# Kernel tuning notes

Hardware: AMD Instinct MI355X
Metric: run time of the kernel (lower is better)

## Reference

```python
import jax, jax.numpy as jnp
import numpy as np

N_QUBITS = 4
INV_SQRT2 = np.float32(1.0 / np.sqrt(2.0))
CNOT_PAIRS = [(0, 1), (1, 2), (2, 3), (3, 0), (0, 2), (1, 3), (2, 0), (3, 1)]


def _apply_1q(state, U, w):
    # state: (B,2,2,2,2); U: (B,2,2) batched or (2,2) shared
    state = jnp.moveaxis(state, w + 1, 1)
    if U.ndim == 3:
        state = jnp.einsum('bij,bj...->bi...', U, state)
    else:
        state = jnp.einsum('ij,bj...->bi...', U, state)
    return jnp.moveaxis(state, 1, w + 1)


def _apply_cnot(state, c, t):
    st = jnp.moveaxis(state, (c + 1, t + 1), (1, 2))
    st = jnp.stack([st[:, 0], st[:, 1, ::-1]], axis=1)  # flip target where ctrl=1
    return jnp.moveaxis(st, (1, 2), (c + 1, t + 1))


def _ry_batched(theta):  # theta: (B,) -> (B,2,2) complex
    c, s = jnp.cos(theta * 0.5), jnp.sin(theta * 0.5)
    return jnp.stack([jnp.stack([c, -s], -1), jnp.stack([s, c], -1)], -2).astype(jnp.complex64)


def _rz_batched(theta):  # theta: (B,) -> (B,2,2) complex (diag(e^{-i t/2}, e^{i t/2}))
    e = jnp.exp(-0.5j * theta.astype(jnp.complex64))
    z = jnp.zeros_like(e)
    return jnp.stack([jnp.stack([e, z], -1), jnp.stack([z, jnp.conj(e)], -1)], -2)


def _ry1(t):  # scalar -> (2,2)
    c, s = jnp.cos(t * 0.5), jnp.sin(t * 0.5)
    return jnp.stack([jnp.stack([c, -s]), jnp.stack([s, c])]).astype(jnp.complex64)


def _rz1(t):  # scalar -> (2,2)
    e = jnp.exp(-0.5j * t.astype(jnp.complex64))
    z = jnp.zeros_like(e)
    return jnp.stack([jnp.stack([e, z]), jnp.stack([z, jnp.conj(e)])])


def _circuit(f, weights):
    # f: (B, 4) angle features; weights: (L, 4, 3). Returns <Z_i> per wire: (B, 4).
    B = f.shape[0]
    state = jnp.zeros((B, 2, 2, 2, 2), jnp.complex64).at[:, 0, 0, 0, 0].set(1.0)
    H = jnp.array([[1.0, 1.0], [1.0, -1.0]], jnp.complex64) * INV_SQRT2
    for i in range(N_QUBITS):
        state = _apply_1q(state, H, i)
        state = _apply_1q(state, _ry_batched(jnp.arctan(f[:, i])), i)
        state = _apply_1q(state, _rz_batched(jnp.arctan(f[:, i] ** 2)), i)
    n_layers = weights.shape[0]
    for l in range(n_layers):
        for c, t in CNOT_PAIRS:
            state = _apply_cnot(state, c, t)
        for i in range(N_QUBITS):
            phi, theta, omega = weights[l, i, 0], weights[l, i, 1], weights[l, i, 2]
            # PennyLane Rot(phi, theta, omega) = RZ(omega) @ RY(theta) @ RZ(phi)
            U = _rz1(omega) @ _ry1(theta) @ _rz1(phi)
            state = _apply_1q(state, U, i)
    probs = jnp.abs(state) ** 2  # (B,2,2,2,2)
    z = []
    for i in range(N_QUBITS):
        axes = tuple(a for a in range(1, N_QUBITS + 1) if a != i + 1)
        m = probs.sum(axes)  # (B,2)
        z.append(m[:, 0] - m[:, 1])
    return jnp.stack(z, -1)


def setup_inputs() -> dict:
    key = jax.random.key(0)
    ks = jax.random.split(key, 6)
    B, D_IN, D_OUT, L = 131072, 256, 64, 2
    x = jax.random.normal(ks[0], (B, D_IN), jnp.float32)
    W1 = jax.random.normal(ks[1], (N_QUBITS, D_IN), jnp.float32) * (1.0 / np.sqrt(D_IN))
    b1 = jax.random.normal(ks[2], (N_QUBITS,), jnp.float32) * 0.1
    weights = jax.random.normal(ks[3], (L, N_QUBITS, 3), jnp.float32)
    W2 = jax.random.normal(ks[4], (D_OUT, N_QUBITS), jnp.float32) * 0.5
    b2 = jax.random.normal(ks[5], (D_OUT,), jnp.float32) * 0.1
    return {"x": x, "W1": W1, "b1": b1, "weights": weights, "W2": W2, "b2": b2}


def reference(x, W1, b1, weights, W2, b2):
    f = jnp.tanh(x @ W1.T + b1) * jnp.pi  # (B,4)
    q = _circuit(f, weights)              # (B,4) expval(PauliZ)
    return q @ W2.T + b2                  # (B, D_OUT)
```

## Files before the change

### kernel.cpp

```cpp
#include <hip/hip_runtime.h>
#include <math.h>

#define NQ 4
#define DIN 256
#define DOUT 64
#define NLAYER 2
#define TPB 256
#define WROWS 64
#define NIT (WROWS/2)
#define PF 3

typedef float nt4 __attribute__((ext_vector_type(4)));

__device__ __forceinline__ float tanh_fast(float y) {
    float e = __expf(2.0f * y);
    return 1.0f - 2.0f / (e + 1.0f);
}

__global__ __launch_bounds__(TPB, 2) void qp_fused(
    const float* __restrict__ x,  const float* __restrict__ W1,
    const float* __restrict__ b1, const float* __restrict__ wts,
    const float* __restrict__ W2, const float* __restrict__ b2,
    float* __restrict__ out)
{
    __shared__ __align__(16) float fs[4][WROWS][NQ];
    __shared__ __align__(16) float qs[4][WROWS][NQ];
    __shared__ __align__(16) float w2s[DOUT][NQ];
    __shared__ __align__(16) float us[8][8];
    __shared__ float b2s[DOUT];

    const int t = threadIdx.x;
    const int wave = t >> 6, lane = t & 63;
    const int half = lane >> 5;
    const int cl   = lane & 31;
    const int qsel = lane & 3;

    if (t < 64) {
        ((float4*)&w2s[0][0])[t] = ((const float4*)W2)[t];
        b2s[t] = b2[t];
    }
    if (t < 8) {
        const float phi = wts[t*3 + 0], th = wts[t*3 + 1], om = wts[t*3 + 2];
        float sth, cth; sincosf(0.5f*th, &sth, &cth);
        float sp, cp;   sincosf(0.5f*(phi+om), &sp, &cp);
        float sm, cm;   sincosf(0.5f*(phi-om), &sm, &cm);
        us[t][0] =  cth*cp; us[t][1] = -cth*sp;
        us[t][2] = -sth*cm; us[t][3] = -sth*sm;
        us[t][4] =  sth*cm; us[t][5] = -sth*sm;
        us[t][6] =  cth*cp; us[t][7] =  cth*sp;
    }
    __syncthreads();

    const int wrow = (blockIdx.x * 4 + wave) * WROWS;
    float (* __restrict__ fsw)[NQ] = fs[wave];
    float (* __restrict__ qsw)[NQ] = qs[wave];

    {
        float4 w[4][2];
        #pragma unroll
        for (int q = 0; q < 4; ++q) {
            w[q][0] = ((const float4*)W1)[q*64 + cl];
            w[q][1] = ((const float4*)W1)[q*64 + 32 + cl];
        }
        const float4 bv = *(const float4*)b1;
        const float bsel = (qsel==0)?bv.x:(qsel==1)?bv.y:(qsel==2)?bv.z:bv.w;

        const int row0 = wrow + half;

        nt4 buf[PF+1][2];
        #pragma unroll
        for (int k = 0; k < PF; ++k) {
            const nt4* xn = (const nt4*)(x + (size_t)(row0 + k*2) * DIN);
            buf[k][0] = __builtin_nontemporal_load(xn + cl);
            buf[k][1] = __builtin_nontemporal_load(xn + 32 + cl);
        }

        #pragma unroll
        for (int it = 0; it < NIT; ++it) {
            if (it + PF < NIT) {
                const nt4* xn = (const nt4*)(x + (size_t)(row0 + (it+PF)*2) * DIN);
                buf[(it+PF)&PF][0] = __builtin_nontemporal_load(xn + cl);
                buf[(it+PF)&PF][1] = __builtin_nontemporal_load(xn + 32 + cl);
            }
            const nt4 xv0 = buf[it&PF][0];
            const nt4 xv1 = buf[it&PF][1];

            float a0, a1, a2, a3;
            a0 = fmaf(xv0.x,w[0][0].x, fmaf(xv0.y,w[0][0].y, fmaf(xv0.z,w[0][0].z, xv0.w*w[0][0].w)));
            a1 = fmaf(xv0.x,w[1][0].x, fmaf(xv0.y,w[1][0].y, fmaf(xv0.z,w[1][0].z, xv0.w*w[1][0].w)));
            a2 = fmaf(xv0.x,w[2][0].x, fmaf(xv0.y,w[2][0].y, fmaf(xv0.z,w[2][0].z, xv0.w*w[2][0].w)));
            a3 = fmaf(xv0.x,w[3][0].x, fmaf(xv0.y,w[3][0].y, fmaf(xv0.z,w[3][0].z, xv0.w*w[3][0].w)));
            a0 = fmaf(xv1.x,w[0][1].x, fmaf(xv1.y,w[0][1].y, fmaf(xv1.z,w[0][1].z, fmaf(xv1.w,w[0][1].w, a0))));
            a1 = fmaf(xv1.x,w[1][1].x, fmaf(xv1.y,w[1][1].y, fmaf(xv1.z,w[1][1].z, fmaf(xv1.w,w[1][1].w, a1))));
            a2 = fmaf(xv1.x,w[2][1].x, fmaf(xv1.y,w[2][1].y, fmaf(xv1.z,w[2][1].z, fmaf(xv1.w,w[2][1].w, a2))));
            a3 = fmaf(xv1.x,w[3][1].x, fmaf(xv1.y,w[3][1].y, fmaf(xv1.z,w[3][1].z, fmaf(xv1.w,w[3][1].w, a3))));

            a0 += __shfl_xor(a0, 1, 64);  a1 += __shfl_xor(a1, 1, 64);
            a2 += __shfl_xor(a2, 1, 64);  a3 += __shfl_xor(a3, 1, 64);
            a0 += __shfl_xor(a0, 2, 64);  a1 += __shfl_xor(a1, 2, 64);
            a2 += __shfl_xor(a2, 2, 64);  a3 += __shfl_xor(a3, 2, 64);
            float v = (qsel==0)?a0:(qsel==1)?a1:(qsel==2)?a2:a3;
            v += __shfl_xor(v, 4, 64);
            v += __shfl_xor(v, 8, 64);
            v += __shfl_xor(v, 16, 64);

            if (cl < 4) {
                const float PI = 3.14159265358979f;
                fsw[it*2 + half][qsel] = PI * tanh_fast(v + bsel);
            }
        }
    }

    {
        const float4 fv = *(const float4*)fsw[lane];
        const float fq[4] = {fv.x, fv.y, fv.z, fv.w};
        const float IS2 = 0.70710678118654752f;
        float vr[4][2], vi[4][2];
        #pragma unroll
        for (int i = 0; i < 4; ++i) {
            const float fi = fq[i];
            const float f2 = fi*fi;
            const float ca = rsqrtf(1.0f + f2);
            const float ch = sqrtf(0.5f*(1.0f + ca));
            const float sh = copysignf(sqrtf(fmaxf(0.5f*(1.0f - ca), 0.0f)), fi);
            const float cb = rsqrtf(1.0f + f2*f2);
            const float cbh = sqrtf(0.5f*(1.0f + cb));
            const float sbh = sqrtf(fmaxf(0.5f*(1.0f - cb), 0.0f));
            const float u0 = (ch - sh) * IS2;
            const float u1 = (ch + sh) * IS2;
            vr[i][0] = u0 * cbh;  vi[i][0] = -u0 * sbh;
            vr[i][1] = u1 * cbh;  vi[i][1] =  u1 * sbh;
        }
        float ar[16], ai[16];
        #pragma unroll
        for (int i0 = 0; i0 < 2; ++i0)
        #pragma unroll
        for (int i1 = 0; i1 < 2; ++i1) {
            const float pr  = vr[0][i0]*vr[1][i1] - vi[0][i0]*vi[1][i1];
            const float pim = vr[0][i0]*vi[1][i1] + vi[0][i0]*vr[1][i1];
            #pragma unroll
            for (int i2 = 0; i2 < 2; ++i2)
            #pragma unroll
            for (int i3 = 0; i3 < 2; ++i3) {
                const float qr  = vr[2][i2]*vr[3][i3] - vi[2][i2]*vi[3][i3];
                const float qim = vr[2][i2]*vi[3][i3] + vi[2][i2]*vr[3][i3];
                const int idx = i0*8 + i1*4 + i2*2 + i3;
                ar[idx] = pr*qr - pim*qim;
                ai[idx] = pr*qim + pim*qr;
            }
        }
        #pragma unroll
        for (int l = 0; l < NLAYER; ++l) {
            constexpr int cpairs[8][2] = {{0,1},{1,2},{2,3},{3,0},{0,2},{1,3},{2,0},{3,1}};
            #pragma unroll
            for (int g = 0; g < 8; ++g) {
                const int bc = 8 >> cpairs[g][0];
                const int bt = 8 >> cpairs[g][1];
                #pragma unroll
                for (int m = 0; m < 16; ++m) {
                    if ((m & bc) && !(m & bt)) {
                        const int m2 = m | bt;
                        float tr = ar[m]; ar[m] = ar[m2]; ar[m2] = tr;
                        float ti = ai[m]; ai[m] = ai[m2]; ai[m2] = ti;
                    }
                }
            }
            #pragma unroll
            for (int i = 0; i < 4; ++i) {
                const float* u = &us[l*4 + i][0];
                const float u00r=u[0], u00i=u[1], u01r=u[2], u01i=u[3];
                const float u10r=u[4], u10i=u[5], u11r=u[6], u11i=u[7];
                const int bq = 8 >> i;
                #pragma unroll
                for (int m = 0; m < 16; ++m) {
                    if (!(m & bq)) {
                        const int m2 = m | bq;
                        const float a0r=ar[m], a0i=ai[m], a1r=ar[m2], a1i=ai[m2];
                        ar[m]  = u00r*a0r - u00i*a0i + u01r*a1r - u01i*a1i;
                        ai[m]  = u00r*a0i + u00i*a0r + u01r*a1i + u01i*a1r;
                        ar[m2] = u10r*a0r - u10i*a0i + u11r*a1r - u11i*a1i;
                        ai[m2] = u10r*a0i + u10i*a0r + u11r*a1i + u11i*a1r;
                    }
                }
            }
        }
        float z0=0.f, z1=0.f, z2=0.f, z3=0.f;
        #pragma unroll
        for (int m = 0; m < 16; ++m) {
            const float p = ar[m]*ar[m] + ai[m]*ai[m];
            z0 += (m & 8) ? -p : p;
            z1 += (m & 4) ? -p : p;
            z2 += (m & 2) ? -p : p;
            z3 += (m & 1) ? -p : p;
        }
        float4 qv; qv.x=z0; qv.y=z1; qv.z=z2; qv.w=z3;
        *(float4*)qsw[lane] = qv;
    }

    {
        const int j4 = lane & 15;
        const int rb = lane >> 4;
        float w2r[4][4], b2r[4];
        #pragma unroll
        for (int jj = 0; jj < 4; ++jj) {
            const int j = j4*4 + jj;
            #pragma unroll
            for (int i = 0; i < 4; ++i) w2r[jj][i] = w2s[j][i];
            b2r[jj] = b2s[j];
        }
        #pragma unroll
        for (int e = 0; e < WROWS/4; ++e) {
            const int r = e*4 + rb;
            const float4 q = *(const float4*)qsw[r];
            nt4 o;
            o.x = fmaf(q.x,w2r[0][0], fmaf(q.y,w2r[0][1], fmaf(q.z,w2r[0][2], fmaf(q.w,w2r[0][3], b2r[0]))));
            o.y = fmaf(q.x,w2r[1][0], fmaf(q.y,w2r[1][1], fmaf(q.z,w2r[1][2], fmaf(q.w,w2r[1][3], b2r[1]))));
            o.z = fmaf(q.x,w2r[2][0], fmaf(q.y,w2r[2][1], fmaf(q.z,w2r[2][2], fmaf(q.w,w2r[2][3], b2r[2]))));
            o.w = fmaf(q.x,w2r[3][0], fmaf(q.y,w2r[3][1], fmaf(q.z,w2r[3][2], fmaf(q.w,w2r[3][3], b2r[3]))));
            __builtin_nontemporal_store(o, (nt4*)(out + (size_t)(wrow + r) * DOUT) + j4);
        }
    }
}

extern "C" void kernel_launch(void* const* d_in, const int* in_sizes, int n_in,
                              void* d_out, int out_size, void* d_ws, size_t ws_size,
                              hipStream_t stream) {
    const float* x  = (const float*)d_in[0];
    const float* W1 = (const float*)d_in[1];
    const float* b1 = (const float*)d_in[2];
    const float* wt = (const float*)d_in[3];
    const float* W2 = (const float*)d_in[4];
    const float* b2 = (const float*)d_in[5];
    float* out = (float*)d_out;
    const int B = in_sizes[0] / DIN;
    qp_fused<<<B / (WROWS * 4), TPB, 0, stream>>>(x, W1, b1, wt, W2, b2, out);
}
```

Before: 35.67 us.

## Split fused kernel into separate projection and circuit/output kernels

Splits the single fused kernel into two launches. The first streams x and computes the tanh projection into a workspace buffer (or into the output buffer as scratch), using many more, smaller blocks. The second does the circuit simulation with one row per thread and the output projection. This raises parallelism and occupancy for the memory-bound read of x and for the compute phase, at the cost of a second launch and an extra global round trip for the features.

```diff
diff --git a/kernel.cpp b/kernel.cpp
--- a/kernel.cpp
+++ b/kernel.cpp
@@ -6,9 +6,8 @@
 #define DOUT 64
 #define NLAYER 2
 #define TPB 256
-#define WROWS 64
-#define NIT (WROWS/2)
 #define PF 3
+#define K1_NIT 8
 
 typedef float nt4 __attribute__((ext_vector_type(4)));
 
@@ -17,28 +16,83 @@
     return 1.0f - 2.0f / (e + 1.0f);
 }
 
-__global__ __launch_bounds__(TPB, 2) void qp_fused(
-    const float* __restrict__ x,  const float* __restrict__ W1,
-    const float* __restrict__ b1, const float* __restrict__ wts,
-    const float* __restrict__ W2, const float* __restrict__ b2,
-    float* __restrict__ out)
+__global__ __launch_bounds__(TPB, 4) void qp_k1(
+    const float* __restrict__ x, const float* __restrict__ W1,
+    const float* __restrict__ b1, float* __restrict__ fbuf, int fstride)
 {
-    __shared__ __align__(16) float fs[4][WROWS][NQ];
-    __shared__ __align__(16) float qs[4][WROWS][NQ];
-    __shared__ __align__(16) float w2s[DOUT][NQ];
-    __shared__ __align__(16) float us[8][8];
-    __shared__ float b2s[DOUT];
-
     const int t = threadIdx.x;
     const int wave = t >> 6, lane = t & 63;
     const int half = lane >> 5;
     const int cl   = lane & 31;
     const int qsel = lane & 3;
 
-    if (t < 64) {
-        ((float4*)&w2s[0][0])[t] = ((const float4*)W2)[t];
-        b2s[t] = b2[t];
-    }
+    float4 w[4][2];
+    #pragma unroll
+    for (int q = 0; q < 4; ++q) {
+        w[q][0] = ((const float4*)W1)[q*64 + cl];
+        w[q][1] = ((const float4*)W1)[q*64 + 32 + cl];
+    }
+    const float4 bv = *(const float4*)b1;
+    const float bsel = (qsel==0)?bv.x:(qsel==1)?bv.y:(qsel==2)?bv.z:bv.w;
+
+    const int wrow = blockIdx.x * 64 + wave * 16;
+    const int row0 = wrow + half;
+
+    nt4 buf[PF+1][2];
+    #pragma unroll
+    for (int k = 0; k < PF; ++k) {
+        const nt4* xn = (const nt4*)(x + (size_t)(row0 + k*2) * DIN);
+        buf[k][0] = __builtin_nontemporal_load(xn + cl);
+        buf[k][1] = __builtin_nontemporal_load(xn + 32 + cl);
+    }
+
+    #pragma unroll
+    for (int it = 0; it < K1_NIT; ++it) {
+        if (it + PF < K1_NIT) {
+            const nt4* xn = (const nt4*)(x + (size_t)(row0 + (it+PF)*2) * DIN);
+            buf[(it+PF)&PF][0] = __builtin_nontemporal_load(xn + cl);
+            buf[(it+PF)&PF][1] = __builtin_nontemporal_load(xn + 32 + cl);
+        }
+        const nt4 xv0 = buf[it&PF][0];
+        const nt4 xv1 = buf[it&PF][1];
+
+        float a0, a1, a2, a3;
+        a0 = fmaf(xv0.x,w[0][0].x, fmaf(xv0.y,w[0][0].y, fmaf(xv0.z,w[0][0].z, xv0.w*w[0][0].w)));
+        a1 = fmaf(xv0.x,w[1][0].x, fmaf(xv0.y,w[1][0].y, fmaf(xv0.z,w[1][0].z, xv0.w*w[1][0].w)));
+        a2 = fmaf(xv0.x,w[2][0].x, fmaf(xv0.y,w[2][0].y, fmaf(xv0.z,w[2][0].z, xv0.w*w[2][0].w)));
+        a3 = fmaf(xv0.x,w[3][0].x, fmaf(xv0.y,w[3][0].y, fmaf(xv0.z,w[3][0].z, xv0.w*w[3][0].w)));
+        a0 = fmaf(xv1.x,w[0][1].x, fmaf(xv1.y,w[0][1].y, fmaf(xv1.z,w[0][1].z, fmaf(xv1.w,w[0][1].w, a0))));
+        a1 = fmaf(xv1.x,w[1][1].x, fmaf(xv1.y,w[1][1].y, fmaf(xv1.z,w[1][1].z, fmaf(xv1.w,w[1][1].w, a1))));
+        a2 = fmaf(xv1.x,w[2][1].x, fmaf(xv1.y,w[2][1].y, fmaf(xv1.z,w[2][1].z, fmaf(xv1.w,w[2][1].w, a2))));
+        a3 = fmaf(xv1.x,w[3][1].x, fmaf(xv1.y,w[3][1].y, fmaf(xv1.z,w[3][1].z, fmaf(xv1.w,w[3][1].w, a3))));
+
+        a0 += __shfl_xor(a0, 1, 64);  a1 += __shfl_xor(a1, 1, 64);
+        a2 += __shfl_xor(a2, 1, 64);  a3 += __shfl_xor(a3, 1, 64);
+        a0 += __shfl_xor(a0, 2, 64);  a1 += __shfl_xor(a1, 2, 64);
+        a2 += __shfl_xor(a2, 2, 64);  a3 += __shfl_xor(a3, 2, 64);
+        float v = (qsel==0)?a0:(qsel==1)?a1:(qsel==2)?a2:a3;
+        v += __shfl_xor(v, 4, 64);
+        v += __shfl_xor(v, 8, 64);
+        v += __shfl_xor(v, 16, 64);
+
+        if (cl < 4) {
+            const float PI = 3.14159265358979f;
+            fbuf[(size_t)(row0 + it*2) * fstride + qsel] = PI * tanh_fast(v + bsel);
+        }
+    }
+}
+
+__global__ __launch_bounds__(TPB, 4) void qp_k2(
+    const float* __restrict__ fbuf, int fstride,
+    const float* __restrict__ wts, const float* __restrict__ W2,
+    const float* __restrict__ b2, float* __restrict__ out)
+{
+    __shared__ __align__(16) float qs[TPB][NQ];
+    __shared__ __align__(16) float us[8][8];
+
+    const int t = threadIdx.x;
+    const int brow = blockIdx.x * TPB;
+
     if (t < 8) {
         const float phi = wts[t*3 + 0], th = wts[t*3 + 1], om = wts[t*3 + 2];
         float sth, cth; sincosf(0.5f*th, &sth, &cth);
@@ -51,68 +105,8 @@
     }
     __syncthreads();
 
-    const int wrow = (blockIdx.x * 4 + wave) * WROWS;
-    float (* __restrict__ fsw)[NQ] = fs[wave];
-    float (* __restrict__ qsw)[NQ] = qs[wave];
-
     {
-        float4 w[4][2];
-        #pragma unroll
-        for (int q = 0; q < 4; ++q) {
-            w[q][0] = ((const float4*)W1)[q*64 + cl];
-            w[q][1] = ((const float4*)W1)[q*64 + 32 + cl];
-        }
-        const float4 bv = *(const float4*)b1;
-        const float bsel = (qsel==0)?bv.x:(qsel==1)?bv.y:(qsel==2)?bv.z:bv.w;
-
-        const int row0 = wrow + half;
-
-        nt4 buf[PF+1][2];
-        #pragma unroll
-        for (int k = 0; k < PF; ++k) {
-            const nt4* xn = (const nt4*)(x + (size_t)(row0 + k*2) * DIN);
-            buf[k][0] = __builtin_nontemporal_load(xn + cl);
-            buf[k][1] = __builtin_nontemporal_load(xn + 32 + cl);
-        }
-
-        #pragma unroll
-        for (int it = 0; it < NIT; ++it) {
-            if (it + PF < NIT) {
-                const nt4* xn = (const nt4*)(x + (size_t)(row0 + (it+PF)*2) * DIN);
-                buf[(it+PF)&PF][0] = __builtin_nontemporal_load(xn + cl);
-                buf[(it+PF)&PF][1] = __builtin_nontemporal_load(xn + 32 + cl);
-            }
-            const nt4 xv0 = buf[it&PF][0];
-            const nt4 xv1 = buf[it&PF][1];
-
-            float a0, a1, a2, a3;
-            a0 = fmaf(xv0.x,w[0][0].x, fmaf(xv0.y,w[0][0].y, fmaf(xv0.z,w[0][0].z, xv0.w*w[0][0].w)));
-            a1 = fmaf(xv0.x,w[1][0].x, fmaf(xv0.y,w[1][0].y, fmaf(xv0.z,w[1][0].z, xv0.w*w[1][0].w)));
-            a2 = fmaf(xv0.x,w[2][0].x, fmaf(xv0.y,w[2][0].y, fmaf(xv0.z,w[2][0].z, xv0.w*w[2][0].w)));
-            a3 = fmaf(xv0.x,w[3][0].x, fmaf(xv0.y,w[3][0].y, fmaf(xv0.z,w[3][0].z, xv0.w*w[3][0].w)));
-            a0 = fmaf(xv1.x,w[0][1].x, fmaf(xv1.y,w[0][1].y, fmaf(xv1.z,w[0][1].z, fmaf(xv1.w,w[0][1].w, a0))));
-            a1 = fmaf(xv1.x,w[1][1].x, fmaf(xv1.y,w[1][1].y, fmaf(xv1.z,w[1][1].z, fmaf(xv1.w,w[1][1].w, a1))));
-            a2 = fmaf(xv1.x,w[2][1].x, fmaf(xv1.y,w[2][1].y, fmaf(xv1.z,w[2][1].z, fmaf(xv1.w,w[2][1].w, a2))));
-            a3 = fmaf(xv1.x,w[3][1].x, fmaf(xv1.y,w[3][1].y, fmaf(xv1.z,w[3][1].z, fmaf(xv1.w,w[3][1].w, a3))));
-
-            a0 += __shfl_xor(a0, 1, 64);  a1 += __shfl_xor(a1, 1, 64);
-            a2 += __shfl_xor(a2, 1, 64);  a3 += __shfl_xor(a3, 1, 64);
-            a0 += __shfl_xor(a0, 2, 64);  a1 += __shfl_xor(a1, 2, 64);
-            a2 += __shfl_xor(a2, 2, 64);  a3 += __shfl_xor(a3, 2, 64);
-            float v = (qsel==0)?a0:(qsel==1)?a1:(qsel==2)?a2:a3;
-            v += __shfl_xor(v, 4, 64);
-            v += __shfl_xor(v, 8, 64);
-            v += __shfl_xor(v, 16, 64);
-
-            if (cl < 4) {
-                const float PI = 3.14159265358979f;
-                fsw[it*2 + half][qsel] = PI * tanh_fast(v + bsel);
-            }
-        }
-    }
-
-    {
-        const float4 fv = *(const float4*)fsw[lane];
+        const float4 fv = *(const float4*)(fbuf + (size_t)(brow + t) * fstride);
         const float fq[4] = {fv.x, fv.y, fv.z, fv.w};
         const float IS2 = 0.70710678118654752f;
         float vr[4][2], vi[4][2];
@@ -194,30 +188,28 @@
             z3 += (m & 1) ? -p : p;
         }
         float4 qv; qv.x=z0; qv.y=z1; qv.z=z2; qv.w=z3;
-        *(float4*)qsw[lane] = qv;
-    }
+        ((float4*)qs)[t] = qv;
+    }
+    __syncthreads();
 
     {
-        const int j4 = lane & 15;
-        const int rb = lane >> 4;
-        float w2r[4][4], b2r[4];
-        #pragma unroll
-        for (int jj = 0; jj < 4; ++jj) {
-            const int j = j4*4 + jj;
-            #pragma unroll
-            for (int i = 0; i < 4; ++i) w2r[jj][i] = w2s[j][i];
-            b2r[jj] = b2s[j];
-        }
-        #pragma unroll
-        for (int e = 0; e < WROWS/4; ++e) {
-            const int r = e*4 + rb;
-            const float4 q = *(const float4*)qsw[r];
+        const int j4 = t & 15;
+        const int rb = t >> 4;
+        float4 w2r[4];
+        #pragma unroll
+        for (int jj = 0; jj < 4; ++jj) w2r[jj] = ((const float4*)W2)[j4*4 + jj];
+        const float4 b2v = ((const float4*)b2)[j4];
+
+        #pragma unroll
+        for (int e = 0; e < TPB/16; ++e) {
+            const int r = e*16 + rb;
+            const float4 q = ((const float4*)qs)[r];
             nt4 o;
-            o.x = fmaf(q.x,w2r[0][0], fmaf(q.y,w2r[0][1], fmaf(q.z,w2r[0][2], fmaf(q.w,w2r[0][3], b2r[0]))));
-            o.y = fmaf(q.x,w2r[1][0], fmaf(q.y,w2r[1][1], fmaf(q.z,w2r[1][2], fmaf(q.w,w2r[1][3], b2r[1]))));
-            o.z = fmaf(q.x,w2r[2][0], fmaf(q.y,w2r[2][1], fmaf(q.z,w2r[2][2], fmaf(q.w,w2r[2][3], b2r[2]))));
-            o.w = fmaf(q.x,w2r[3][0], fmaf(q.y,w2r[3][1], fmaf(q.z,w2r[3][2], fmaf(q.w,w2r[3][3], b2r[3]))));
-            __builtin_nontemporal_store(o, (nt4*)(out + (size_t)(wrow + r) * DOUT) + j4);
+            o.x = fmaf(q.x,w2r[0].x, fmaf(q.y,w2r[0].y, fmaf(q.z,w2r[0].z, fmaf(q.w,w2r[0].w, b2v.x))));
+            o.y = fmaf(q.x,w2r[1].x, fmaf(q.y,w2r[1].y, fmaf(q.z,w2r[1].z, fmaf(q.w,w2r[1].w, b2v.y))));
+            o.z = fmaf(q.x,w2r[2].x, fmaf(q.y,w2r[2].y, fmaf(q.z,w2r[2].z, fmaf(q.w,w2r[2].w, b2v.z))));
+            o.w = fmaf(q.x,w2r[3].x, fmaf(q.y,w2r[3].y, fmaf(q.z,w2r[3].z, fmaf(q.w,w2r[3].w, b2v.w))));
+            __builtin_nontemporal_store(o, (nt4*)(out + (size_t)(brow + r) * DOUT) + j4);
         }
     }
 }
@@ -233,5 +225,15 @@
     const float* b2 = (const float*)d_in[5];
     float* out = (float*)d_out;
     const int B = in_sizes[0] / DIN;
-    qp_fused<<<B / (WROWS * 4), TPB, 0, stream>>>(x, W1, b1, wt, W2, b2, out);
-}
+
+    float* fbuf;
+    int fstride;
+    if (ws_size >= (size_t)B * NQ * sizeof(float)) {
+        fbuf = (float*)d_ws; fstride = NQ;
+    } else {
+        fbuf = out; fstride = DOUT;
+    }
+
+    qp_k1<<<B / 64, TPB, 0, stream>>>(x, W1, b1, fbuf, fstride);
+    qp_k2<<<B / TPB, TPB, 0, stream>>>(fbuf, fstride, wt, W2, b2, out);
+}
```

New measurement: 41.38 us. 16.0% more time.
